# Performance work log

Hardware: AMD Instinct MI355X
Metric: run time of the kernel (lower is better)

The kernel has to match this reference:

```python
import jax, jax.numpy as jnp
import numpy as np

D = 768
H = 12
B, T = 2, 2048


def _layernorm(x, g, b, eps=1e-5):
    m = jnp.mean(x, axis=-1, keepdims=True)
    v = jnp.mean((x - m) ** 2, axis=-1, keepdims=True)
    return (x - m) * jax.lax.rsqrt(v + eps) * g + b


def setup_inputs() -> dict:
    key = jax.random.key(0)
    ks = jax.random.split(key, 10)
    s = 0.02
    return {
        "x": jax.random.normal(ks[0], (B, T, D), dtype=jnp.float32),
        "attn_mask": jnp.ones((B, T), dtype=jnp.int32),
        "Wq": jax.random.normal(ks[1], (D, D), dtype=jnp.float32) * s,
        "Wk": jax.random.normal(ks[2], (D, D), dtype=jnp.float32) * s,
        "Wv": jax.random.normal(ks[3], (D, D), dtype=jnp.float32) * s,
        "Wo": jax.random.normal(ks[4], (D, D), dtype=jnp.float32) * s,
        "bo": jnp.zeros((D,), dtype=jnp.float32),
        "ln1_g": jnp.ones((D,), dtype=jnp.float32),
        "ln1_b": jnp.zeros((D,), dtype=jnp.float32),
        "ln2_g": jnp.ones((D,), dtype=jnp.float32),
        "ln2_b": jnp.zeros((D,), dtype=jnp.float32),
        "W1": jax.random.normal(ks[5], (D, 4 * D), dtype=jnp.float32) * s,
        "b1": jnp.zeros((4 * D,), dtype=jnp.float32),
        "W2": jax.random.normal(ks[6], (4 * D, D), dtype=jnp.float32) * s,
        "b2": jnp.zeros((D,), dtype=jnp.float32),
    }


def reference(x, attn_mask, Wq, Wk, Wv, Wo, bo, ln1_g, ln1_b, ln2_g, ln2_b, W1, b1, W2, b2):
    d = x.shape[-1]
    hs = d // H
    # --- multi-head self-attention on ln1(x) ---
    h = _layernorm(x, ln1_g, ln1_b)
    q = jnp.einsum("btd,dhk->bhtk", h, Wq.reshape(d, H, hs))
    k = jnp.einsum("btd,dhk->bhtk", h, Wk.reshape(d, H, hs))
    v = jnp.einsum("btd,dhk->bhtk", h, Wv.reshape(d, H, hs))
    # NOTE: original scales by embed_dim**-0.5 (C = embed_dim), not head_size
    scores = jnp.einsum("bhtk,bhsk->bhts", q, k) * (d ** -0.5)
    key_mask = (attn_mask == 0)[:, None, None, :]  # [B,1,1,T] over key dim
    scores = jnp.where(key_mask, -jnp.inf, scores)
    wei = jax.nn.softmax(scores, axis=-1)
    out = jnp.einsum("bhts,bhsk->bhtk", wei, v)
    out = out.transpose(0, 2, 1, 3).reshape(x.shape)  # concat heads -> [B,T,D]
    x = x + out @ Wo + bo
    # --- feed-forward on ln2(x) ---
    h2 = _layernorm(x, ln2_g, ln2_b)
    ff = jax.nn.relu(h2 @ W1 + b1) @ W2 + b2
    return x + ff
```

## Files before the change

kernel.cpp:

```cpp
#include <hip/hip_runtime.h>
#include <hip/hip_bf16.h>


typedef unsigned short u16;
typedef unsigned int u32;
typedef __attribute__((ext_vector_type(8))) short s16x8;
typedef __attribute__((ext_vector_type(4))) short s16x4;
typedef __attribute__((ext_vector_type(4))) float fx4;

#define D_MODEL 768
#define NH 12
#define HS 64
#define TT 2048
#define BB 2

__device__ __forceinline__ u16 f2bf(float f) {
  union { float f; u32 u; } v; v.f = f;
  u32 r = v.u + 0x7fffu + ((v.u >> 16) & 1u);
  return (u16)(r >> 16);
}
__device__ __forceinline__ float bf2f(u16 h) {
  union { u32 u; float f; } v; v.u = ((u32)h) << 16; return v.f;
}
__device__ __forceinline__ s16x4 pack4(float a, float b, float c, float d) {
  union { __hip_bfloat162 h2[2]; s16x4 v; } u;
  u.h2[0] = __float22bfloat162_rn({a, b});
  u.h2[1] = __float22bfloat162_rn({c, d});
  return u.v;
}

__device__ __forceinline__ void async16(const void* g, void* l) {
  __builtin_amdgcn_global_load_lds(
      (const __attribute__((address_space(1))) u32*)g,
      (__attribute__((address_space(3))) u32*)l, 16, 0, 0);
}

__global__ __launch_bounds__(256) void preproc(
    const float* __restrict__ x, const int* __restrict__ mask,
    const float* __restrict__ Wq, const float* __restrict__ Wk,
    const float* __restrict__ Wv, const float* __restrict__ Wo,
    const float* __restrict__ W1, const float* __restrict__ W2,
    const float* __restrict__ g1, const float* __restrict__ be1,
    u16* __restrict__ WqkvT, u16* __restrict__ WoT,
    u16* __restrict__ W1T, u16* __restrict__ W2T,
    u16* __restrict__ h1, float* __restrict__ mb) {
  __shared__ float t[32][33];
  __shared__ float ss[4], ssq[4];
  const int bid = blockIdx.x, tid = threadIdx.x;
  if (bid < 6912) {
    const float* in; u16* out; int R, C, cx, cy;
    if (bid < 1728) {
      int wsel = bid / 576, s = bid % 576;
      in = wsel == 0 ? Wq : wsel == 1 ? Wk : Wv;
      out = WqkvT + (size_t)wsel * 768 * 768;
      R = 768; C = 768; cx = s % 24; cy = s / 24;
    } else if (bid < 2304) {
      int s = bid - 1728; in = Wo; out = WoT;
      R = 768; C = 768; cx = s % 24; cy = s / 24;
    } else if (bid < 4608) {
      int s = bid - 2304; in = W1; out = W1T;
      R = 768; C = 3072; cx = s % 96; cy = s / 96;
    } else {
      int s = bid - 4608; in = W2; out = W2T;
      R = 3072; C = 768; cx = s % 24; cy = s / 24;
    }
    int c0 = cx * 32, r0 = cy * 32, xx = tid & 31, yy = tid >> 5;
    for (int i = 0; i < 4; i++)
      t[yy + i * 8][xx] = in[(size_t)(r0 + yy + i * 8) * C + c0 + xx];
    __syncthreads();
    for (int i = 0; i < 4; i++)
      out[(size_t)(c0 + yy + i * 8) * R + r0 + xx] = f2bf(t[xx][yy + i * 8]);
  } else if (bid < 11008) {
    int row = bid - 6912;
    const float* xr = x + (size_t)row * D_MODEL;
    float v0 = xr[tid], v1 = xr[tid + 256], v2 = xr[tid + 512];
    float s = v0 + v1 + v2, sq = v0 * v0 + v1 * v1 + v2 * v2;
    for (int m = 1; m < 64; m <<= 1) { s += __shfl_xor(s, m); sq += __shfl_xor(sq, m); }
    int w = tid >> 6;
    if ((tid & 63) == 0) { ss[w] = s; ssq[w] = sq; }
    __syncthreads();
    s = ss[0] + ss[1] + ss[2] + ss[3];
    sq = ssq[0] + ssq[1] + ssq[2] + ssq[3];
    float mean = s * (1.f / D_MODEL);
    float var = sq * (1.f / D_MODEL) - mean * mean;
    float rstd = rsqrtf(var + 1e-5f);
    u16* orow = h1 + (size_t)row * D_MODEL;
    orow[tid]       = f2bf((v0 - mean) * rstd * g1[tid]       + be1[tid]);
    orow[tid + 256] = f2bf((v1 - mean) * rstd * g1[tid + 256] + be1[tid + 256]);
    orow[tid + 512] = f2bf((v2 - mean) * rstd * g1[tid + 512] + be1[tid + 512]);
  } else {
    int i = (bid - 11008) * 256 + tid;
    mb[i] = mask[i] ? 0.f : -1e30f;
  }
}

__global__ __launch_bounds__(256) void red_wo_ln(
    const u16* __restrict__ p0, const u16* __restrict__ p1,
    const float* __restrict__ x, const float* __restrict__ bo,
    const float* __restrict__ g, const float* __restrict__ be,
    float* __restrict__ yv, u16* __restrict__ h2) {
  int row = blockIdx.x, tid = threadIdx.x;
  size_t base = (size_t)row * D_MODEL;
  float v[3];
  float s = 0.f, sq = 0.f;
  for (int i = 0; i < 3; i++) {
    int c = tid + i * 256;
    size_t idx = base + c;
    float t = bf2f(p0[idx]) + bf2f(p1[idx]) + x[idx] + bo[c];
    v[i] = t; yv[idx] = t;
    s += t; sq += t * t;
  }
  for (int m = 1; m < 64; m <<= 1) { s += __shfl_xor(s, m); sq += __shfl_xor(sq, m); }
  __shared__ float ss[4], ssq[4];
  int w = tid >> 6;
  if ((tid & 63) == 0) { ss[w] = s; ssq[w] = sq; }
  __syncthreads();
  s = ss[0] + ss[1] + ss[2] + ss[3];
  sq = ssq[0] + ssq[1] + ssq[2] + ssq[3];
  float mean = s * (1.f / D_MODEL);
  float var = sq * (1.f / D_MODEL) - mean * mean;
  float rstd = rsqrtf(var + 1e-5f);
  for (int i = 0; i < 3; i++) {
    int c = tid + i * 256;
    h2[base + c] = f2bf((v[i] - mean) * rstd * g[c] + be[c]);
  }
}

__global__ __launch_bounds__(256) void red_ff2(
    const u16* __restrict__ p0, const u16* __restrict__ p1,
    const float* __restrict__ yv,
    const float* __restrict__ bias, float* __restrict__ out) {
  size_t i = ((size_t)blockIdx.x * 256 + threadIdx.x) * 4;
  int col = (int)(i % D_MODEL);
  ushort4 a = *(const ushort4*)(p0 + i);
  ushort4 b = *(const ushort4*)(p1 + i);
  float4 y = *(const float4*)(yv + i);
  float4 o;
  o.x = bf2f(a.x) + bf2f(b.x) + y.x + bias[col];
  o.y = bf2f(a.y) + bf2f(b.y) + y.y + bias[col + 1];
  o.z = bf2f(a.z) + bf2f(b.z) + y.z + bias[col + 2];
  o.w = bf2f(a.w) + bf2f(b.w) + y.w + bias[col + 3];
  *(float4*)(out + i) = o;
}

template <int EPI>
__global__ __launch_bounds__(256) void gemm_bt(
    const u16* __restrict__ A, const u16* __restrict__ Bt,
    int M, int N, int K,
    u16* __restrict__ outb, const float* __restrict__ bias,
    float qs, u16* __restrict__ vtp,
    u16* __restrict__ p0, u16* __restrict__ p1) {
  __shared__ __align__(16) u16 lA[64 * 64];
  __shared__ __align__(16) u16 lB[128 * 64];
  const int tid = threadIdx.x;
  const int lane = tid & 63, w = tid >> 6;
  const int quad = lane >> 4, l15 = lane & 15;
  const int wm = w >> 1, wn = w & 1;
  const int bm = blockIdx.y, bn = blockIdx.x;
  const int Ksub = K / gridDim.z;
  const int k0 = blockIdx.z * Ksub;

  fx4 acc[2][4] = {};

  for (int kt = k0; kt < k0 + Ksub; kt += 64) {
    __syncthreads();
    #pragma unroll
    for (int t = 0; t < 2; t++) {
      int p = t * 256 + tid;
      int m = p >> 3, qp = p & 7, ql = qp ^ (m & 7);
      async16(A + (size_t)(bm * 64 + m) * K + kt + ql * 8,
              (char*)lA + t * 4096 + w * 1024);
    }
    #pragma unroll
    for (int t = 0; t < 4; t++) {
      int p = t * 256 + tid;
      int n = p >> 3, qp = p & 7, ql = qp ^ (n & 7);
      async16(Bt + (size_t)(bn * 128 + n) * K + kt + ql * 8,
              (char*)lB + t * 4096 + w * 1024);
    }
    __syncthreads();
    #pragma unroll
    for (int kk = 0; kk < 2; kk++) {
      s16x8 af[2], bfr[4];
      #pragma unroll
      for (int i = 0; i < 2; i++) {
        int m = wm * 32 + i * 16 + l15;
        af[i] = *(const s16x8*)((const char*)lA + m * 128 +
                                (((kk * 4 + quad) ^ (m & 7)) * 16));
      }
      #pragma unroll
      for (int j = 0; j < 4; j++) {
        int n = wn * 64 + j * 16 + l15;
        bfr[j] = *(const s16x8*)((const char*)lB + n * 128 +
                                 (((kk * 4 + quad) ^ (n & 7)) * 16));
      }
      #pragma unroll
      for (int i = 0; i < 2; i++)
        #pragma unroll
        for (int j = 0; j < 4; j++)
          acc[i][j] = __builtin_amdgcn_mfma_f32_16x16x32_bf16(af[i], bfr[j], acc[i][j], 0, 0, 0);
    }
  }

  u16* pb = (EPI == 3) ? (blockIdx.z == 0 ? p0 : p1) : nullptr;

  #pragma unroll
  for (int i = 0; i < 2; i++)
    #pragma unroll
    for (int j = 0; j < 4; j++) {
      int row0 = bm * 64 + wm * 32 + i * 16 + quad * 4;
      int col = bn * 128 + wn * 64 + j * 16 + l15;
      if (EPI == 0) {
        if (vtp != nullptr && col >= 1536) {
          int bb = row0 >> 11, t0 = row0 & 2047;
          ushort4 pk = {f2bf(acc[i][j][0]), f2bf(acc[i][j][1]),
                        f2bf(acc[i][j][2]), f2bf(acc[i][j][3])};
          *(ushort4*)(vtp + ((size_t)(bb * 768 + (col - 1536)) << 11) + t0) = pk;
        } else {
          float sc = (col < 768) ? qs : 1.f;
          for (int r = 0; r < 4; r++)
            outb[(size_t)(row0 + r) * N + col] = f2bf(acc[i][j][r] * sc);
        }
      } else if (EPI == 2) {
        for (int r = 0; r < 4; r++)
          outb[(size_t)(row0 + r) * N + col] = f2bf(fmaxf(acc[i][j][r] + bias[col], 0.f));
      } else {
        for (int r = 0; r < 4; r++)
          pb[(size_t)(row0 + r) * N + col] = f2bf(acc[i][j][r]);
      }
    }
}

__global__ __launch_bounds__(512) void attn_kernel(
    const u16* __restrict__ qkv, const u16* __restrict__ vt,
    const float* __restrict__ maskadd,
    u16* __restrict__ pO0, u16* __restrict__ pO1, float* __restrict__ pL) {
  __shared__ __align__(16) u16 sQ[128 * 64];
  __shared__ __align__(16) u16 sK[128 * 64];
  __shared__ __align__(16) u16 sV[64 * 132];
  __shared__ __align__(16) float smask[1024];
  const int bh = blockIdx.y, b = bh / NH, h = bh % NH;
  const int qt = blockIdx.x, sp = blockIdx.z;
  const int tid = threadIdx.x, lane = tid & 63, w = tid >> 6;
  const int quad = lane >> 4, l15 = lane & 15;

  for (int i = 0; i < 2; i++) {
    int p = i * 512 + tid;
    int m = p >> 3, qp = p & 7, ql = qp ^ (m & 7);
    async16(qkv + (size_t)(b * TT + qt * 128 + m) * 2304 + h * HS + ql * 8,
            (char*)sQ + i * 8192 + w * 1024);
  }
  smask[tid]       = maskadd[b * TT + sp * 1024 + tid];
  smask[tid + 512] = maskadd[b * TT + sp * 1024 + 512 + tid];
  const u16* vbase = vt + (size_t)bh * HS * TT + (size_t)(tid >> 3) * TT + sp * 1024;
  s16x8 vc0 = *(const s16x8*)(vbase + (tid & 7) * 16);
  s16x8 vc1 = *(const s16x8*)(vbase + (tid & 7) * 16 + 8);
  __syncthreads();

  const int qrow = w * 16 + l15;
  s16x8 aq0 = *(const s16x8*)((const char*)sQ + qrow * 128 + ((quad ^ (l15 & 7)) * 16));
  s16x8 aq1 = *(const s16x8*)((const char*)sQ + qrow * 128 + (((4 + quad) ^ (l15 & 7)) * 16));

  const char* pK0 = (const char*)sK + l15 * 128 + ((quad ^ (l15 & 7)) * 16);
  const char* pK1 = (const char*)sK + l15 * 128 + (((4 + quad) ^ (l15 & 7)) * 16);
  const char* pV  = (const char*)sV + l15 * 264 + quad * 8;
  char* vwr = (char*)sV + (tid >> 3) * 264 + (tid & 7) * 32;

  float lsum = 0.f;
  fx4 o[4] = {};

  for (int kc = 0; kc < 8; kc++) {
    __syncthreads();
    #pragma unroll
    for (int i = 0; i < 2; i++) {
      int p = i * 512 + tid;
      int m = p >> 3, qp = p & 7, ql = qp ^ (m & 7);
      async16(qkv + (size_t)(b * TT + sp * 1024 + kc * 128 + m) * 2304 + D_MODEL + h * HS + ql * 8,
              (char*)sK + i * 8192 + w * 1024);
    }
    *(s16x8*)vwr = vc0;
    *(s16x8*)(vwr + 16) = vc1;
    __syncthreads();
    int kn = (kc < 7 ? kc + 1 : kc) * 128;
    s16x8 vn0 = *(const s16x8*)(vbase + kn + (tid & 7) * 16);
    s16x8 vn1 = *(const s16x8*)(vbase + kn + (tid & 7) * 16 + 8);

    #pragma unroll
    for (int kt = 0; kt < 8; kt++) {
      float4 mb = *(const float4*)&smask[kc * 128 + kt * 16 + quad * 4];
      fx4 s = {mb.x, mb.y, mb.z, mb.w};
      s16x8 ak0 = *(const s16x8*)(pK0 + kt * 2048);
      s16x8 ak1 = *(const s16x8*)(pK1 + kt * 2048);
      s = __builtin_amdgcn_mfma_f32_16x16x32_bf16(ak0, aq0, s, 0, 0, 0);
      s = __builtin_amdgcn_mfma_f32_16x16x32_bf16(ak1, aq1, s, 0, 0, 0);
      float e0 = __builtin_amdgcn_exp2f(s[0]);
      float e1 = __builtin_amdgcn_exp2f(s[1]);
      float e2 = __builtin_amdgcn_exp2f(s[2]);
      float e3 = __builtin_amdgcn_exp2f(s[3]);
      lsum += (e0 + e1) + (e2 + e3);
      s16x4 pB = pack4(e0, e1, e2, e3);
      #pragma unroll
      for (int jv = 0; jv < 4; jv++) {
        s16x4 av = *(const s16x4*)(pV + jv * 4224 + kt * 32);
        o[jv] = __builtin_amdgcn_mfma_f32_16x16x16bf16_1k(av, pB, o[jv], 0, 0, 0);
      }
    }
    vc0 = vn0; vc1 = vn1;
  }

  lsum += __shfl_xor(lsum, 16);
  lsum += __shfl_xor(lsum, 32);

  const int tile = bh * 32 + qt * 2 + (w >> 2);
  const int sub = (w & 3) * 16;
  u16* po = sp ? pO1 : pO0;
  size_t base = (size_t)tile * 4096;
  for (int jv = 0; jv < 4; jv++)
    for (int r = 0; r < 4; r++) {
      int vd = jv * 16 + quad * 4 + r;
      po[base + vd * 64 + sub + l15] = f2bf(o[jv][r]);
    }
  if (quad == 0) pL[sp * 49152 + tile * 64 + sub + l15] = lsum;
}

__global__ __launch_bounds__(256) void attn_reduce(
    const u16* __restrict__ pO0, const u16* __restrict__ pO1,
    const float* __restrict__ pL, u16* __restrict__ out) {
  __shared__ float T[64 * 65];
  __shared__ float rinv[64];
  const int tile = blockIdx.x;
  const int bh = tile >> 5, qt = tile & 31, b = bh / NH, h = bh % NH;
  const int t = threadIdx.x;
  if (t < 64) rinv[t] = 1.f / (pL[tile * 64 + t] + pL[49152 + tile * 64 + t]);
  __syncthreads();
  size_t base = (size_t)tile * 4096;
  for (int i = 0; i < 16; i++) {
    int idx = i * 256 + t, vd = idx >> 6, q = idx & 63;
    T[vd * 65 + q] = (bf2f(pO0[base + idx]) + bf2f(pO1[base + idx])) * rinv[q];
  }
  __syncthreads();
  int q = t >> 2, vb = (t & 3) * 16;
  u16* orow = out + (size_t)(b * TT + qt * 64 + q) * D_MODEL + h * HS + vb;
  for (int i = 0; i < 8; i++) {
    int vd = vb + i * 2;
    u32 pk = (u32)f2bf(T[vd * 65 + q]) | ((u32)f2bf(T[(vd + 1) * 65 + q]) << 16);
    *(u32*)(orow + i * 2) = pk;
  }
}

extern "C" void kernel_launch(void* const* d_in, const int* in_sizes, int n_in,
                              void* d_out, int out_size, void* d_ws, size_t ws_size,
                              hipStream_t stream) {
  const float* x    = (const float*)d_in[0];
  const int*   mask = (const int*)d_in[1];
  const float* Wq   = (const float*)d_in[2];
  const float* Wk   = (const float*)d_in[3];
  const float* Wv   = (const float*)d_in[4];
  const float* Wo   = (const float*)d_in[5];
  const float* bo   = (const float*)d_in[6];
  const float* g1   = (const float*)d_in[7];
  const float* be1  = (const float*)d_in[8];
  const float* g2   = (const float*)d_in[9];
  const float* be2  = (const float*)d_in[10];
  const float* W1   = (const float*)d_in[11];
  const float* bb1  = (const float*)d_in[12];
  const float* W2   = (const float*)d_in[13];
  const float* bb2  = (const float*)d_in[14];
  float* out = (float*)d_out;
  char* ws = (char*)d_ws;

  u16*   WqkvT = (u16*)(ws + 0);
  u16*   WoT   = (u16*)(ws + 3538944);
  u16*   W1T   = (u16*)(ws + 4718592);
  u16*   W2T   = (u16*)(ws + 9437184);
  u16*   h1    = (u16*)(ws + 14155776);
  u16*   QKV   = (u16*)(ws + 20447232);
  u16*   Vt    = (u16*)(ws + 39321600);
  u16*   attn  = (u16*)(ws + 45613056);
  float* yv    = (float*)(ws + 51904512);
  float* mbias = yv;
  u16*   pO0   = h1;
  u16*   pO1   = (u16*)(ws + 51920896);
  float* pL    = (float*)(ws + 58212352);
  u16*   h2    = h1;
  u16*   ff1   = QKV;
  u16* pw0 = (u16*)(ws + 20447232);
  u16* pw1 = (u16*)(ws + 26738688);
  u16* pf0 = (u16*)(ws + 0);
  u16* pf1 = (u16*)(ws + 14155776);

  const float QS = 0.05205875399f;

  preproc<<<11024, 256, 0, stream>>>(x, mask, Wq, Wk, Wv, Wo, W1, W2,
                                     g1, be1, WqkvT, WoT, W1T, W2T, h1, mbias);
  gemm_bt<0><<<dim3(18, 64, 1), 256, 0, stream>>>(h1, WqkvT, 4096, 2304, 768,
      QKV, nullptr, QS, Vt, nullptr, nullptr);
  attn_kernel<<<dim3(16, 24, 2), 512, 0, stream>>>(QKV, Vt, mbias, pO0, pO1, pL);
  attn_reduce<<<768, 256, 0, stream>>>(pO0, pO1, pL, attn);
  gemm_bt<3><<<dim3(6, 64, 2), 256, 0, stream>>>(attn, WoT, 4096, 768, 768,
      nullptr, nullptr, 1.f, nullptr, pw0, pw1);
  red_wo_ln<<<4096, 256, 0, stream>>>(pw0, pw1, x, bo, g2, be2, yv, h2);
  gemm_bt<2><<<dim3(24, 64, 1), 256, 0, stream>>>(h2, W1T, 4096, 3072, 768,
      ff1, bb1, 1.f, nullptr, nullptr, nullptr);
  gemm_bt<3><<<dim3(6, 64, 2), 256, 0, stream>>>(ff1, W2T, 4096, 768, 3072,
      nullptr, nullptr, 1.f, nullptr, pf0, pf1);
  red_ff2<<<3072, 256, 0, stream>>>(pf0, pf1, yv, bb2, out);
}
```

Baseline: 270.8 us.

## Split attention keys four ways instead of two with smaller K/V chunks

The attention kernel now splits each query tile's 2048 keys into four 512-key partitions, using 64-key chunks per loop iteration instead of 128. This doubles the grid to 1536 blocks and shrinks per-block LDS so more blocks can be resident. The reduce kernel sums four partial outputs and row sums, and workspace buffers are reassigned to hold the extra partials. The cost is more partial-output traffic, a heavier reduce, and more barriers per key processed.

```diff
diff --git a/kernel.cpp b/kernel.cpp
--- a/kernel.cpp
+++ b/kernel.cpp
@@ -234,11 +234,12 @@
 __global__ __launch_bounds__(512) void attn_kernel(
     const u16* __restrict__ qkv, const u16* __restrict__ vt,
     const float* __restrict__ maskadd,
-    u16* __restrict__ pO0, u16* __restrict__ pO1, float* __restrict__ pL) {
+    u16* __restrict__ pO0, u16* __restrict__ pO1,
+    u16* __restrict__ pO2, u16* __restrict__ pO3, float* __restrict__ pL) {
   __shared__ __align__(16) u16 sQ[128 * 64];
-  __shared__ __align__(16) u16 sK[128 * 64];
-  __shared__ __align__(16) u16 sV[64 * 132];
-  __shared__ __align__(16) float smask[1024];
+  __shared__ __align__(16) u16 sK[64 * 64];
+  __shared__ __align__(16) u16 sV[64 * 68];
+  __shared__ __align__(16) float smask[512];
   const int bh = blockIdx.y, b = bh / NH, h = bh % NH;
   const int qt = blockIdx.x, sp = blockIdx.z;
   const int tid = threadIdx.x, lane = tid & 63, w = tid >> 6;
@@ -250,11 +251,9 @@
     async16(qkv + (size_t)(b * TT + qt * 128 + m) * 2304 + h * HS + ql * 8,
             (char*)sQ + i * 8192 + w * 1024);
   }
-  smask[tid]       = maskadd[b * TT + sp * 1024 + tid];
-  smask[tid + 512] = maskadd[b * TT + sp * 1024 + 512 + tid];
-  const u16* vbase = vt + (size_t)bh * HS * TT + (size_t)(tid >> 3) * TT + sp * 1024;
-  s16x8 vc0 = *(const s16x8*)(vbase + (tid & 7) * 16);
-  s16x8 vc1 = *(const s16x8*)(vbase + (tid & 7) * 16 + 8);
+  smask[tid & 511] = maskadd[b * TT + sp * 512 + (tid & 511)];
+  const u16* vbase = vt + (size_t)bh * HS * TT + (size_t)(tid >> 3) * TT + sp * 512;
+  s16x8 vcur = *(const s16x8*)(vbase + (tid & 7) * 8);
   __syncthreads();
 
   const int qrow = w * 16 + l15;
@@ -263,31 +262,27 @@
 
   const char* pK0 = (const char*)sK + l15 * 128 + ((quad ^ (l15 & 7)) * 16);
   const char* pK1 = (const char*)sK + l15 * 128 + (((4 + quad) ^ (l15 & 7)) * 16);
-  const char* pV  = (const char*)sV + l15 * 264 + quad * 8;
-  char* vwr = (char*)sV + (tid >> 3) * 264 + (tid & 7) * 32;
+  const char* pV  = (const char*)sV + l15 * 136 + quad * 8;
+  char* vwr = (char*)sV + (tid >> 3) * 136 + (tid & 7) * 16;
 
   float lsum = 0.f;
   fx4 o[4] = {};
 
   for (int kc = 0; kc < 8; kc++) {
     __syncthreads();
+    {
+      int m = tid >> 3, qp = tid & 7, ql = qp ^ (m & 7);
+      async16(qkv + (size_t)(b * TT + sp * 512 + kc * 64 + m) * 2304 + D_MODEL + h * HS + ql * 8,
+              (char*)sK + w * 1024);
+    }
+    *(s16x8*)vwr = vcur;
+    __syncthreads();
+    int kn = (kc < 7 ? kc + 1 : kc) * 64;
+    s16x8 vnxt = *(const s16x8*)(vbase + kn + (tid & 7) * 8);
+
     #pragma unroll
-    for (int i = 0; i < 2; i++) {
-      int p = i * 512 + tid;
-      int m = p >> 3, qp = p & 7, ql = qp ^ (m & 7);
-      async16(qkv + (size_t)(b * TT + sp * 1024 + kc * 128 + m) * 2304 + D_MODEL + h * HS + ql * 8,
-              (char*)sK + i * 8192 + w * 1024);
-    }
-    *(s16x8*)vwr = vc0;
-    *(s16x8*)(vwr + 16) = vc1;
-    __syncthreads();
-    int kn = (kc < 7 ? kc + 1 : kc) * 128;
-    s16x8 vn0 = *(const s16x8*)(vbase + kn + (tid & 7) * 16);
-    s16x8 vn1 = *(const s16x8*)(vbase + kn + (tid & 7) * 16 + 8);
-
-    #pragma unroll
-    for (int kt = 0; kt < 8; kt++) {
-      float4 mb = *(const float4*)&smask[kc * 128 + kt * 16 + quad * 4];
+    for (int kt = 0; kt < 4; kt++) {
+      float4 mb = *(const float4*)&smask[kc * 64 + kt * 16 + quad * 4];
       fx4 s = {mb.x, mb.y, mb.z, mb.w};
       s16x8 ak0 = *(const s16x8*)(pK0 + kt * 2048);
       s16x8 ak1 = *(const s16x8*)(pK1 + kt * 2048);
@@ -301,11 +296,11 @@
       s16x4 pB = pack4(e0, e1, e2, e3);
       #pragma unroll
       for (int jv = 0; jv < 4; jv++) {
-        s16x4 av = *(const s16x4*)(pV + jv * 4224 + kt * 32);
+        s16x4 av = *(const s16x4*)(pV + jv * 2176 + kt * 32);
         o[jv] = __builtin_amdgcn_mfma_f32_16x16x16bf16_1k(av, pB, o[jv], 0, 0, 0);
       }
     }
-    vc0 = vn0; vc1 = vn1;
+    vcur = vnxt;
   }
 
   lsum += __shfl_xor(lsum, 16);
@@ -313,7 +308,7 @@
 
   const int tile = bh * 32 + qt * 2 + (w >> 2);
   const int sub = (w & 3) * 16;
-  u16* po = sp ? pO1 : pO0;
+  u16* po = sp == 0 ? pO0 : sp == 1 ? pO1 : sp == 2 ? pO2 : pO3;
   size_t base = (size_t)tile * 4096;
   for (int jv = 0; jv < 4; jv++)
     for (int r = 0; r < 4; r++) {
@@ -325,18 +320,23 @@
 
 __global__ __launch_bounds__(256) void attn_reduce(
     const u16* __restrict__ pO0, const u16* __restrict__ pO1,
+    const u16* __restrict__ pO2, const u16* __restrict__ pO3,
     const float* __restrict__ pL, u16* __restrict__ out) {
   __shared__ float T[64 * 65];
   __shared__ float rinv[64];
   const int tile = blockIdx.x;
   const int bh = tile >> 5, qt = tile & 31, b = bh / NH, h = bh % NH;
   const int t = threadIdx.x;
-  if (t < 64) rinv[t] = 1.f / (pL[tile * 64 + t] + pL[49152 + tile * 64 + t]);
+  if (t < 64) {
+    int i = tile * 64 + t;
+    rinv[t] = 1.f / (pL[i] + pL[49152 + i] + pL[98304 + i] + pL[147456 + i]);
+  }
   __syncthreads();
   size_t base = (size_t)tile * 4096;
   for (int i = 0; i < 16; i++) {
     int idx = i * 256 + t, vd = idx >> 6, q = idx & 63;
-    T[vd * 65 + q] = (bf2f(pO0[base + idx]) + bf2f(pO1[base + idx])) * rinv[q];
+    T[vd * 65 + q] = (bf2f(pO0[base + idx]) + bf2f(pO1[base + idx]) +
+                      bf2f(pO2[base + idx]) + bf2f(pO3[base + idx])) * rinv[q];
   }
   __syncthreads();
   int q = t >> 2, vb = (t & 3) * 16;
@@ -376,18 +376,20 @@
   u16*   h1    = (u16*)(ws + 14155776);
   u16*   QKV   = (u16*)(ws + 20447232);
   u16*   Vt    = (u16*)(ws + 39321600);
-  u16*   attn  = (u16*)(ws + 45613056);
+  float* mbias = (float*)(ws + 64487424);
+  u16*   pO0   = h1;
+  u16*   pO1   = (u16*)(ws + 45613056);
+  u16*   pO2   = (u16*)(ws + 51904512);
+  u16*   pO3   = (u16*)(ws + 58195968);
+  float* pL    = (float*)(ws + 0);
+  u16*   attnO = QKV;
+  u16*   pw0   = (u16*)(ws + 26738688);
+  u16*   pw1   = (u16*)(ws + 33030144);
   float* yv    = (float*)(ws + 51904512);
-  float* mbias = yv;
-  u16*   pO0   = h1;
-  u16*   pO1   = (u16*)(ws + 51920896);
-  float* pL    = (float*)(ws + 58212352);
   u16*   h2    = h1;
   u16*   ff1   = QKV;
-  u16* pw0 = (u16*)(ws + 20447232);
-  u16* pw1 = (u16*)(ws + 26738688);
-  u16* pf0 = (u16*)(ws + 0);
-  u16* pf1 = (u16*)(ws + 14155776);
+  u16*   pf0   = (u16*)(ws + 0);
+  u16*   pf1   = (u16*)(ws + 14155776);
 
   const float QS = 0.05205875399f;
 
@@ -395,9 +397,10 @@
                                      g1, be1, WqkvT, WoT, W1T, W2T, h1, mbias);
   gemm_bt<0><<<dim3(18, 64, 1), 256, 0, stream>>>(h1, WqkvT, 4096, 2304, 768,
       QKV, nullptr, QS, Vt, nullptr, nullptr);
-  attn_kernel<<<dim3(16, 24, 2), 512, 0, stream>>>(QKV, Vt, mbias, pO0, pO1, pL);
-  attn_reduce<<<768, 256, 0, stream>>>(pO0, pO1, pL, attn);
-  gemm_bt<3><<<dim3(6, 64, 2), 256, 0, stream>>>(attn, WoT, 4096, 768, 768,
+  attn_kernel<<<dim3(16, 24, 4), 512, 0, stream>>>(QKV, Vt, mbias,
+      pO0, pO1, pO2, pO3, pL);
+  attn_reduce<<<768, 256, 0, stream>>>(pO0, pO1, pO2, pO3, pL, attnO);
+  gemm_bt<3><<<dim3(6, 64, 2), 256, 0, stream>>>(attnO, WoT, 4096, 768, 768,
       nullptr, nullptr, 1.f, nullptr, pw0, pw1);
   red_wo_ln<<<4096, 256, 0, stream>>>(pw0, pw1, x, bo, g2, be2, yv, h2);
   gemm_bt<2><<<dim3(24, 64, 1), 256, 0, stream>>>(h2, W1T, 4096, 3072, 768,
```

Measured after the change: 282.6 us. 1.04x slower.

## Drop attention split-K and fuse normalization into single attention kernel

Applied to the files above, without the earlier changes.

The attention kernel now gives each 256-thread block 64 query rows and has it walk all 2048 keys in 64-key chunks. It normalizes by the row sum and writes the concatenated-head output directly. This removes the two-way key split, the partial bf16 output buffers and the separate attn_reduce launch. The mask bias is stored as bf16 to halve its footprint in LDS. In exchange each block runs four times as many serial loop iterations with smaller chunks and more barriers, and the grid keeps the same 768 blocks but with half the threads each.

```diff
diff --git a/kernel.cpp b/kernel.cpp
--- a/kernel.cpp
+++ b/kernel.cpp
@@ -43,7 +43,7 @@
     const float* __restrict__ g1, const float* __restrict__ be1,
     u16* __restrict__ WqkvT, u16* __restrict__ WoT,
     u16* __restrict__ W1T, u16* __restrict__ W2T,
-    u16* __restrict__ h1, float* __restrict__ mb) {
+    u16* __restrict__ h1, u16* __restrict__ mb) {
   __shared__ float t[32][33];
   __shared__ float ss[4], ssq[4];
   const int bid = blockIdx.x, tid = threadIdx.x;
@@ -90,7 +90,7 @@
     orow[tid + 512] = f2bf((v2 - mean) * rstd * g1[tid + 512] + be1[tid + 512]);
   } else {
     int i = (bid - 11008) * 256 + tid;
-    mb[i] = mask[i] ? 0.f : -1e30f;
+    mb[i] = mask[i] ? (u16)0 : f2bf(-1e30f);
   }
 }
 
@@ -231,30 +231,33 @@
     }
 }
 
-__global__ __launch_bounds__(512) void attn_kernel(
+__global__ __launch_bounds__(256) void attn_kernel(
     const u16* __restrict__ qkv, const u16* __restrict__ vt,
-    const float* __restrict__ maskadd,
-    u16* __restrict__ pO0, u16* __restrict__ pO1, float* __restrict__ pL) {
-  __shared__ __align__(16) u16 sQ[128 * 64];
-  __shared__ __align__(16) u16 sK[128 * 64];
-  __shared__ __align__(16) u16 sV[64 * 132];
-  __shared__ __align__(16) float smask[1024];
+    const u16* __restrict__ maskadd, u16* __restrict__ out) {
+  __shared__ __align__(16) u16 sQ[64 * 64];
+  __shared__ __align__(16) u16 sK[64 * 64];
+  __shared__ __align__(16) u16 sV[64 * 68];
+  __shared__ __align__(16) u16 smask[2048];
   const int bh = blockIdx.y, b = bh / NH, h = bh % NH;
-  const int qt = blockIdx.x, sp = blockIdx.z;
+  const int qt = blockIdx.x;
   const int tid = threadIdx.x, lane = tid & 63, w = tid >> 6;
   const int quad = lane >> 4, l15 = lane & 15;
 
+  #pragma unroll
   for (int i = 0; i < 2; i++) {
-    int p = i * 512 + tid;
+    int p = i * 256 + tid;
     int m = p >> 3, qp = p & 7, ql = qp ^ (m & 7);
-    async16(qkv + (size_t)(b * TT + qt * 128 + m) * 2304 + h * HS + ql * 8,
-            (char*)sQ + i * 8192 + w * 1024);
-  }
-  smask[tid]       = maskadd[b * TT + sp * 1024 + tid];
-  smask[tid + 512] = maskadd[b * TT + sp * 1024 + 512 + tid];
-  const u16* vbase = vt + (size_t)bh * HS * TT + (size_t)(tid >> 3) * TT + sp * 1024;
-  s16x8 vc0 = *(const s16x8*)(vbase + (tid & 7) * 16);
-  s16x8 vc1 = *(const s16x8*)(vbase + (tid & 7) * 16 + 8);
+    async16(qkv + (size_t)(b * TT + qt * 64 + m) * 2304 + h * HS + ql * 8,
+            (char*)sQ + i * 4096 + w * 1024);
+  }
+  #pragma unroll
+  for (int j = 0; j < 8; j++)
+    smask[j * 256 + tid] = maskadd[b * TT + j * 256 + tid];
+  const int vr = tid >> 3, vc = tid & 7;
+  const u16* vb0 = vt + ((size_t)bh * HS + vr) * TT;
+  const u16* vb1 = vt + ((size_t)bh * HS + vr + 32) * TT;
+  s16x8 vcur0 = *(const s16x8*)(vb0 + vc * 8);
+  s16x8 vcur1 = *(const s16x8*)(vb1 + vc * 8);
   __syncthreads();
 
   const int qrow = w * 16 + l15;
@@ -263,32 +266,33 @@
 
   const char* pK0 = (const char*)sK + l15 * 128 + ((quad ^ (l15 & 7)) * 16);
   const char* pK1 = (const char*)sK + l15 * 128 + (((4 + quad) ^ (l15 & 7)) * 16);
-  const char* pV  = (const char*)sV + l15 * 264 + quad * 8;
-  char* vwr = (char*)sV + (tid >> 3) * 264 + (tid & 7) * 32;
+  const char* pV  = (const char*)sV + l15 * 136 + quad * 8;
+  char* vw0 = (char*)sV + vr * 136 + vc * 16;
+  char* vw1 = vw0 + 32 * 136;
 
   float lsum = 0.f;
   fx4 o[4] = {};
 
-  for (int kc = 0; kc < 8; kc++) {
+  for (int kc = 0; kc < 32; kc++) {
     __syncthreads();
     #pragma unroll
     for (int i = 0; i < 2; i++) {
-      int p = i * 512 + tid;
+      int p = i * 256 + tid;
       int m = p >> 3, qp = p & 7, ql = qp ^ (m & 7);
-      async16(qkv + (size_t)(b * TT + sp * 1024 + kc * 128 + m) * 2304 + D_MODEL + h * HS + ql * 8,
-              (char*)sK + i * 8192 + w * 1024);
-    }
-    *(s16x8*)vwr = vc0;
-    *(s16x8*)(vwr + 16) = vc1;
-    __syncthreads();
-    int kn = (kc < 7 ? kc + 1 : kc) * 128;
-    s16x8 vn0 = *(const s16x8*)(vbase + kn + (tid & 7) * 16);
-    s16x8 vn1 = *(const s16x8*)(vbase + kn + (tid & 7) * 16 + 8);
-
-    #pragma unroll
-    for (int kt = 0; kt < 8; kt++) {
-      float4 mb = *(const float4*)&smask[kc * 128 + kt * 16 + quad * 4];
-      fx4 s = {mb.x, mb.y, mb.z, mb.w};
+      async16(qkv + (size_t)(b * TT + kc * 64 + m) * 2304 + D_MODEL + h * HS + ql * 8,
+              (char*)sK + i * 4096 + w * 1024);
+    }
+    *(s16x8*)vw0 = vcur0;
+    *(s16x8*)vw1 = vcur1;
+    __syncthreads();
+    int kn = (kc < 31 ? kc + 1 : kc) * 64;
+    s16x8 vn0 = *(const s16x8*)(vb0 + kn + vc * 8);
+    s16x8 vn1 = *(const s16x8*)(vb1 + kn + vc * 8);
+
+    #pragma unroll
+    for (int kt = 0; kt < 4; kt++) {
+      ushort4 mk = *(const ushort4*)&smask[kc * 64 + kt * 16 + quad * 4];
+      fx4 s = {bf2f(mk.x), bf2f(mk.y), bf2f(mk.z), bf2f(mk.w)};
       s16x8 ak0 = *(const s16x8*)(pK0 + kt * 2048);
       s16x8 ak1 = *(const s16x8*)(pK1 + kt * 2048);
       s = __builtin_amdgcn_mfma_f32_16x16x32_bf16(ak0, aq0, s, 0, 0, 0);
@@ -301,51 +305,36 @@
       s16x4 pB = pack4(e0, e1, e2, e3);
       #pragma unroll
       for (int jv = 0; jv < 4; jv++) {
-        s16x4 av = *(const s16x4*)(pV + jv * 4224 + kt * 32);
+        s16x4 av = *(const s16x4*)(pV + jv * 2176 + kt * 32);
         o[jv] = __builtin_amdgcn_mfma_f32_16x16x16bf16_1k(av, pB, o[jv], 0, 0, 0);
       }
     }
-    vc0 = vn0; vc1 = vn1;
+    vcur0 = vn0; vcur1 = vn1;
   }
 
   lsum += __shfl_xor(lsum, 16);
   lsum += __shfl_xor(lsum, 32);
-
-  const int tile = bh * 32 + qt * 2 + (w >> 2);
-  const int sub = (w & 3) * 16;
-  u16* po = sp ? pO1 : pO0;
-  size_t base = (size_t)tile * 4096;
+  float rinv = 1.f / lsum;
+
+  __syncthreads();
+  u16* sT = sV;
+  #pragma unroll
   for (int jv = 0; jv < 4; jv++)
+    #pragma unroll
     for (int r = 0; r < 4; r++) {
       int vd = jv * 16 + quad * 4 + r;
-      po[base + vd * 64 + sub + l15] = f2bf(o[jv][r]);
-    }
-  if (quad == 0) pL[sp * 49152 + tile * 64 + sub + l15] = lsum;
-}
-
-__global__ __launch_bounds__(256) void attn_reduce(
-    const u16* __restrict__ pO0, const u16* __restrict__ pO1,
-    const float* __restrict__ pL, u16* __restrict__ out) {
-  __shared__ float T[64 * 65];
-  __shared__ float rinv[64];
-  const int tile = blockIdx.x;
-  const int bh = tile >> 5, qt = tile & 31, b = bh / NH, h = bh % NH;
-  const int t = threadIdx.x;
-  if (t < 64) rinv[t] = 1.f / (pL[tile * 64 + t] + pL[49152 + tile * 64 + t]);
+      sT[vd * 68 + w * 16 + l15] = f2bf(o[jv][r] * rinv);
+    }
   __syncthreads();
-  size_t base = (size_t)tile * 4096;
-  for (int i = 0; i < 16; i++) {
-    int idx = i * 256 + t, vd = idx >> 6, q = idx & 63;
-    T[vd * 65 + q] = (bf2f(pO0[base + idx]) + bf2f(pO1[base + idx])) * rinv[q];
-  }
-  __syncthreads();
-  int q = t >> 2, vb = (t & 3) * 16;
-  u16* orow = out + (size_t)(b * TT + qt * 64 + q) * D_MODEL + h * HS + vb;
-  for (int i = 0; i < 8; i++) {
-    int vd = vb + i * 2;
-    u32 pk = (u32)f2bf(T[vd * 65 + q]) | ((u32)f2bf(T[(vd + 1) * 65 + q]) << 16);
-    *(u32*)(orow + i * 2) = pk;
-  }
+  int q = tid >> 2, c = tid & 3;
+  u16* orow = out + (size_t)(b * TT + qt * 64 + q) * D_MODEL + h * HS + c * 16;
+  s16x8 o0, o1;
+  #pragma unroll
+  for (int i = 0; i < 8; i++) o0[i] = (short)sT[(c * 16 + i) * 68 + q];
+  #pragma unroll
+  for (int i = 0; i < 8; i++) o1[i] = (short)sT[(c * 16 + 8 + i) * 68 + q];
+  *(s16x8*)orow = o0;
+  *(s16x8*)(orow + 8) = o1;
 }
 
 extern "C" void kernel_launch(void* const* d_in, const int* in_sizes, int n_in,
@@ -378,10 +367,7 @@
   u16*   Vt    = (u16*)(ws + 39321600);
   u16*   attn  = (u16*)(ws + 45613056);
   float* yv    = (float*)(ws + 51904512);
-  float* mbias = yv;
-  u16*   pO0   = h1;
-  u16*   pO1   = (u16*)(ws + 51920896);
-  float* pL    = (float*)(ws + 58212352);
+  u16*   mbias = (u16*)(ws + 51904512);
   u16*   h2    = h1;
   u16*   ff1   = QKV;
   u16* pw0 = (u16*)(ws + 20447232);
@@ -395,8 +381,7 @@
                                      g1, be1, WqkvT, WoT, W1T, W2T, h1, mbias);
   gemm_bt<0><<<dim3(18, 64, 1), 256, 0, stream>>>(h1, WqkvT, 4096, 2304, 768,
       QKV, nullptr, QS, Vt, nullptr, nullptr);
-  attn_kernel<<<dim3(16, 24, 2), 512, 0, stream>>>(QKV, Vt, mbias, pO0, pO1, pL);
-  attn_reduce<<<768, 256, 0, stream>>>(pO0, pO1, pL, attn);
+  attn_kernel<<<dim3(32, 24), 256, 0, stream>>>(QKV, Vt, mbias, attn);
   gemm_bt<3><<<dim3(6, 64, 2), 256, 0, stream>>>(attn, WoT, 4096, 768, 768,
       nullptr, nullptr, 1.f, nullptr, pw0, pw1);
   red_wo_ln<<<4096, 256, 0, stream>>>(pw0, pw1, x, bo, g2, be2, yv, h2);
```

New measurement: 284.7 us. 5.1% more time.
